# Kernel tuning notes

Hardware: AMD Instinct MI355X
Metric: run time of the kernel (lower is better)

Reference implementation:

```python
import jax, jax.numpy as jnp
import numpy as np

B, C, H, W = 8192, 2048, 2, 2
CR = C // 16
EPS = 1e-5

def setup_inputs() -> dict:
    key = jax.random.key(0)
    ks = jax.random.split(key, 8)
    x = jax.random.normal(ks[0], (B, C, H, W), dtype=jnp.float32)
    gamma = jax.random.normal(ks[1], (C,), dtype=jnp.float32) * 0.1 + 1.0
    beta = jax.random.normal(ks[2], (C,), dtype=jnp.float32) * 0.1
    mean = jax.random.normal(ks[3], (C,), dtype=jnp.float32) * 0.1
    var = jax.random.uniform(ks[4], (C,), dtype=jnp.float32, minval=0.5, maxval=1.5)
    w1 = jax.random.normal(ks[5], (CR, C), dtype=jnp.float32) * (1.0 / np.sqrt(C))
    b1 = jnp.zeros((CR,), dtype=jnp.float32)
    w2 = jax.random.normal(ks[6], (C, CR), dtype=jnp.float32) * (1.0 / np.sqrt(CR))
    b2 = jnp.zeros((C,), dtype=jnp.float32)
    return {"x": x, "gamma": gamma, "beta": beta, "mean": mean, "var": var,
            "w1": w1, "b1": b1, "w2": w2, "b2": b2}

def reference(x, gamma, beta, mean, var, w1, b1, w2, b2):
    # BatchNorm (inference form) + ReLU, over [B,C,H,W]
    inv = gamma * jax.lax.rsqrt(var + EPS)           # [C]
    xn = jax.nn.relu(x * inv[None, :, None, None]
                     + (beta - mean * inv)[None, :, None, None])
    # global average pool -> [B, C]
    p = jnp.mean(xn, axis=(2, 3))
    # two 1x1 convs on [B,C,1,1] == channel MLP
    h = jax.nn.relu(jnp.einsum('bc,rc->br', p, w1) + b1)   # [B, C/16]
    g = jax.nn.sigmoid(jnp.einsum('br,cr->bc', h, w2) + b2) # [B, C]
    # repeat(1,1,2,2) then in-place add == broadcast add over 2x2 spatial
    return x + g[:, :, None, None]
```

## Files before the change

kernel.cpp:

```cpp
#include <hip/hip_runtime.h>


typedef unsigned short u16;
typedef unsigned int u32;
typedef short short8 __attribute__((ext_vector_type(8)));
typedef __bf16 bf16x8 __attribute__((ext_vector_type(8)));
typedef unsigned short ushort4v __attribute__((ext_vector_type(4)));
typedef float floatx4 __attribute__((ext_vector_type(4)));

#define C_CH 2048
#define THREADS 512
#define NB_G 16
#define NB_M 8
#define PROW 2056
#define HROW 136

#define WS_W2_OFF   (128 * 2048)
#define WS_B1_BYTE  (1u << 20)
#define WS_G_BYTE   (2u << 20)
#define WS_SMALL_NEED ((size_t)(1u << 20) + 512 + 2048 * 4)
#define WS_FULL_NEED  ((size_t)(2u << 20) + (size_t)8192 * 2048 * 2)

__device__ __forceinline__ float bf2f(u16 u) {
    u32 v = ((u32)u) << 16;
    return __builtin_bit_cast(float, v);
}
__device__ __forceinline__ u16 f2bf(float f) {
    u32 v = __builtin_bit_cast(u32, f);
    v = (v + 0x7FFFu + ((v >> 16) & 1u)) >> 16;
    return (u16)v;
}
__device__ __forceinline__ bf16x8 ld8(const u16* p) {
    short8 s = *(const short8*)p;
    return __builtin_bit_cast(bf16x8, s);
}
__device__ __forceinline__ bool is_bf16_data(const u16* var_raw) {
    int ok = 1;
    #pragma unroll
    for (int i = 0; i < 8; ++i) {
        u16 u = var_raw[2 * i];
        ok &= (u >= 0x3F00u) && (u <= 0x3FC0u);
    }
    return ok != 0;
}

extern "C" __global__ void __launch_bounds__(256)
se_convw(const void* __restrict__ w1_raw, const void* __restrict__ b1_raw,
         const void* __restrict__ w2_raw, const void* __restrict__ b2_raw,
         const void* __restrict__ var_raw, void* __restrict__ ws) {
    const bool bf = is_bf16_data((const u16*)var_raw);
    u16* w1b = (u16*)ws;
    u16* w2b = w1b + WS_W2_OFF;
    float* b1f = (float*)((char*)ws + WS_B1_BYTE);
    float* b2f = b1f + 128;
    int gid = blockIdx.x * 256 + threadIdx.x;
    if (bf) {
        const ushort4v* s1 = (const ushort4v*)w1_raw;
        const ushort4v* s2 = (const ushort4v*)w2_raw;
        *(ushort4v*)(w1b + gid * 4) = s1[gid];
        *(ushort4v*)(w2b + gid * 4) = s2[gid];
        if (gid < 128)  b1f[gid] = bf2f(((const u16*)b1_raw)[gid]);
        if (gid < 2048) b2f[gid] = bf2f(((const u16*)b2_raw)[gid]);
    } else {
        const floatx4* s1 = (const floatx4*)w1_raw;
        const floatx4* s2 = (const floatx4*)w2_raw;
        floatx4 a = s1[gid], b = s2[gid];
        ushort4v o1, o2;
        #pragma unroll
        for (int j = 0; j < 4; ++j) { o1[j] = f2bf(a[j]); o2[j] = f2bf(b[j]); }
        *(ushort4v*)(w1b + gid * 4) = o1;
        *(ushort4v*)(w2b + gid * 4) = o2;
        if (gid < 128)  b1f[gid] = ((const float*)b1_raw)[gid];
        if (gid < 2048) b2f[gid] = ((const float*)b2_raw)[gid];
    }
}

extern "C" __global__ void __launch_bounds__(THREADS, 4)
se_gate(const void* __restrict__ x_raw,
        const void* __restrict__ gamma_raw,
        const void* __restrict__ beta_raw,
        const void* __restrict__ mean_raw,
        const void* __restrict__ var_raw,
        void* __restrict__ ws) {
    __shared__ u16 p_lds[NB_G * PROW];
    __shared__ u16 h_lds[NB_G * HROW];

    const int tid  = threadIdx.x;
    const int lane = tid & 63;
    const int wv   = tid >> 6;
    const int quad = lane >> 4;
    const int l16  = lane & 15;
    const long b0  = (long)blockIdx.x * NB_G;

    const u16*   w1b = (const u16*)ws;
    const u16*   w2b = w1b + WS_W2_OFF;
    const float* b1f = (const float*)((const char*)ws + WS_B1_BYTE);
    const float* b2f = b1f + 128;
    u16*         g_ws = (u16*)((char*)ws + WS_G_BYTE);

    const bool bf = is_bf16_data((const u16*)var_raw);

    {
        float inv[4], bs[4];
        if (bf) {
            const u16 *gu = (const u16*)gamma_raw, *bu = (const u16*)beta_raw,
                      *mu = (const u16*)mean_raw,  *vu = (const u16*)var_raw;
            #pragma unroll
            for (int k = 0; k < 4; ++k) {
                int c = tid + 512 * k;
                float g = bf2f(gu[c]), bb = bf2f(bu[c]);
                float mm = bf2f(mu[c]), vv = bf2f(vu[c]);
                inv[k] = g * rsqrtf(vv + 1e-5f);
                bs[k]  = bb - mm * inv[k];
            }
        } else {
            const float *gf = (const float*)gamma_raw, *bfp = (const float*)beta_raw,
                        *mf = (const float*)mean_raw,  *vf = (const float*)var_raw;
            #pragma unroll
            for (int k = 0; k < 4; ++k) {
                int c = tid + 512 * k;
                inv[k] = gf[c] * rsqrtf(vf[c] + 1e-5f);
                bs[k]  = bfp[c] - mf[c] * inv[k];
            }
        }
        if (bf) {
            const ushort4v* xr = (const ushort4v*)x_raw + b0 * 2048;
            #pragma unroll 2
            for (int m = 0; m < NB_G; ++m) {
                #pragma unroll
                for (int k = 0; k < 4; ++k) {
                    int c = tid + 512 * k;
                    ushort4v u = xr[m * 2048 + c];
                    float s = 0.f;
                    #pragma unroll
                    for (int j = 0; j < 4; ++j)
                        s += fmaxf(fmaf(bf2f(u[j]), inv[k], bs[k]), 0.f);
                    p_lds[m * PROW + c] = f2bf(s * 0.25f);
                }
            }
        } else {
            const floatx4* xr = (const floatx4*)x_raw + b0 * 2048;
            #pragma unroll 2
            for (int m = 0; m < NB_G; ++m) {
                #pragma unroll
                for (int k = 0; k < 4; ++k) {
                    int c = tid + 512 * k;
                    floatx4 v = xr[m * 2048 + c];
                    float s = 0.f;
                    #pragma unroll
                    for (int j = 0; j < 4; ++j)
                        s += fmaxf(fmaf(v[j], inv[k], bs[k]), 0.f);
                    p_lds[m * PROW + c] = f2bf(s * 0.25f);
                }
            }
        }
    }
    __syncthreads();

    const int rr = (wv << 4) | l16;
    {
        floatx4 acc = {0.f, 0.f, 0.f, 0.f};
        const u16* pp  = p_lds + l16 * PROW + (quad << 3);
        const u16* w1p = w1b + (long)rr * C_CH + (quad << 3);
        #pragma unroll 4
        for (int k0 = 0; k0 < C_CH; k0 += 32)
            acc = __builtin_amdgcn_mfma_f32_16x16x32_bf16(ld8(pp + k0), ld8(w1p + k0), acc, 0, 0, 0);
        float bb = b1f[rr];
        #pragma unroll
        for (int r = 0; r < 4; ++r) {
            int m = (quad << 2) | r;
            h_lds[m * HROW + rr] = f2bf(fmaxf(acc[r] + bb, 0.f));
        }
    }
    __syncthreads();

    {
        bf16x8 af[4];
        #pragma unroll
        for (int kk = 0; kk < 4; ++kk)
            af[kk] = ld8(h_lds + l16 * HROW + (kk << 5) + (quad << 3));

        #pragma unroll 2
        for (int i = 0; i < 16; ++i) {
            int c = (wv * 16 + i) * 16 + l16;
            floatx4 a2 = {0.f, 0.f, 0.f, 0.f};
            const u16* w2p = w2b + (long)c * 128 + (quad << 3);
            #pragma unroll
            for (int kk = 0; kk < 4; ++kk)
                a2 = __builtin_amdgcn_mfma_f32_16x16x32_bf16(af[kk], ld8(w2p + (kk << 5)), a2, 0, 0, 0);
            float zb = b2f[c];
            #pragma unroll
            for (int r = 0; r < 4; ++r) {
                int m = (quad << 2) | r;
                float z = a2[r] + zb;
                float g = 1.f / (1.f + __expf(-z));
                g_ws[(b0 + m) * 2048 + c] = f2bf(g);
            }
        }
    }
}

extern "C" __global__ void __launch_bounds__(THREADS)
se_resid(const void* __restrict__ x_raw,
         const void* __restrict__ var_raw,
         const void* __restrict__ ws,
         void* __restrict__ out_raw) {
    const bool bf = is_bf16_data((const u16*)var_raw);
    const u16* g_ws = (const u16*)((const char*)ws + WS_G_BYTE);
    const int tid = threadIdx.x;

    if (bf) {
        const short8* xr  = (const short8*)x_raw;
        short8*       orr = (short8*)out_raw;
        const long base = (long)blockIdx.x * 4096;
        #pragma unroll 4
        for (int it = 0; it < 8; ++it) {
            long j = base + it * 512 + tid;
            u32 gg = *(const u32*)(g_ws + j * 2);
            float g0 = bf2f((u16)gg), g1 = bf2f((u16)(gg >> 16));
            short8 xv = xr[j];
            short8 ov;
            #pragma unroll
            for (int jj = 0; jj < 4; ++jj) ov[jj] = (short)f2bf(bf2f((u16)xv[jj]) + g0);
            #pragma unroll
            for (int jj = 4; jj < 8; ++jj) ov[jj] = (short)f2bf(bf2f((u16)xv[jj]) + g1);
            __builtin_nontemporal_store(ov, &orr[j]);
        }
    } else {
        const floatx4* xr  = (const floatx4*)x_raw;
        floatx4*       orr = (floatx4*)out_raw;
        const long base = (long)blockIdx.x * 8192;
        #pragma unroll 4
        for (int it = 0; it < 16; ++it) {
            long j = base + it * 512 + tid;
            float g = bf2f(g_ws[j]);
            floatx4 xv = xr[j];
            floatx4 ov = {xv[0] + g, xv[1] + g, xv[2] + g, xv[3] + g};
            __builtin_nontemporal_store(ov, &orr[j]);
        }
    }
}

extern "C" __global__ void __launch_bounds__(THREADS, 8)
se_main(const void* __restrict__ x_raw,
        const void* __restrict__ gamma_raw,
        const void* __restrict__ beta_raw,
        const void* __restrict__ mean_raw,
        const void* __restrict__ var_raw,
        const void* __restrict__ ws,
        void* __restrict__ out_raw) {
    __shared__ u16 p_lds[NB_M * PROW];
    __shared__ u16 h_lds[NB_M * HROW];

    const int tid  = threadIdx.x;
    const int lane = tid & 63;
    const int wv   = tid >> 6;
    const int quad = lane >> 4;
    const int l16  = lane & 15;
    const long b0  = (long)blockIdx.x * NB_M;

    const u16*   w1b = (const u16*)ws;
    const u16*   w2b = w1b + WS_W2_OFF;
    const float* b1f = (const float*)((const char*)ws + WS_B1_BYTE);
    const float* b2f = b1f + 128;

    const bool bf = is_bf16_data((const u16*)var_raw);

    {
        float inv[4], bs[4];
        if (bf) {
            const u16 *gu = (const u16*)gamma_raw, *bu = (const u16*)beta_raw,
                      *mu = (const u16*)mean_raw,  *vu = (const u16*)var_raw;
            #pragma unroll
            for (int k = 0; k < 4; ++k) {
                int c = tid + 512 * k;
                float g = bf2f(gu[c]), bb = bf2f(bu[c]);
                float mm = bf2f(mu[c]), vv = bf2f(vu[c]);
                inv[k] = g * rsqrtf(vv + 1e-5f);
                bs[k]  = bb - mm * inv[k];
            }
        } else {
            const float *gf = (const float*)gamma_raw, *bfp = (const float*)beta_raw,
                        *mf = (const float*)mean_raw,  *vf = (const float*)var_raw;
            #pragma unroll
            for (int k = 0; k < 4; ++k) {
                int c = tid + 512 * k;
                inv[k] = gf[c] * rsqrtf(vf[c] + 1e-5f);
                bs[k]  = bfp[c] - mf[c] * inv[k];
            }
        }
        if (bf) {
            const ushort4v* xr = (const ushort4v*)x_raw + b0 * 2048;
            #pragma unroll 2
            for (int m = 0; m < NB_M; ++m) {
                #pragma unroll
                for (int k = 0; k < 4; ++k) {
                    int c = tid + 512 * k;
                    ushort4v u = xr[m * 2048 + c];
                    float s = 0.f;
                    #pragma unroll
                    for (int j = 0; j < 4; ++j)
                        s += fmaxf(fmaf(bf2f(u[j]), inv[k], bs[k]), 0.f);
                    p_lds[m * PROW + c] = f2bf(s * 0.25f);
                }
            }
        } else {
            const floatx4* xr = (const floatx4*)x_raw + b0 * 2048;
            #pragma unroll 2
            for (int m = 0; m < NB_M; ++m) {
                #pragma unroll
                for (int k = 0; k < 4; ++k) {
                    int c = tid + 512 * k;
                    floatx4 v = xr[m * 2048 + c];
                    float s = 0.f;
                    #pragma unroll
                    for (int j = 0; j < 4; ++j)
                        s += fmaxf(fmaf(v[j], inv[k], bs[k]), 0.f);
                    p_lds[m * PROW + c] = f2bf(s * 0.25f);
                }
            }
        }
    }
    __syncthreads();

    const int rr = (wv << 4) | l16;
    {
        floatx4 acc = {0.f, 0.f, 0.f, 0.f};
        const u16* pp  = p_lds + (l16 & 7) * PROW + (quad << 3);
        const u16* w1p = w1b + (long)rr * C_CH + (quad << 3);
        #pragma unroll 4
        for (int k0 = 0; k0 < C_CH; k0 += 32)
            acc = __builtin_amdgcn_mfma_f32_16x16x32_bf16(ld8(pp + k0), ld8(w1p + k0), acc, 0, 0, 0);
        float bb = b1f[rr];
        if (quad < 2) {
            #pragma unroll
            for (int r = 0; r < 4; ++r) {
                int m = (quad << 2) | r;
                h_lds[m * HROW + rr] = f2bf(fmaxf(acc[r] + bb, 0.f));
            }
        }
    }
    __syncthreads();

    {
        bf16x8 af[4];
        #pragma unroll
        for (int kk = 0; kk < 4; ++kk)
            af[kk] = ld8(h_lds + (l16 & 7) * HROW + (kk << 5) + (quad << 3));

        #pragma unroll 2
        for (int i = 0; i < 16; ++i) {
            int c = (wv * 16 + i) * 16 + l16;
            floatx4 a2 = {0.f, 0.f, 0.f, 0.f};
            const u16* w2p = w2b + (long)c * 128 + (quad << 3);
            #pragma unroll
            for (int kk = 0; kk < 4; ++kk)
                a2 = __builtin_amdgcn_mfma_f32_16x16x32_bf16(af[kk], ld8(w2p + (kk << 5)), a2, 0, 0, 0);
            float zb = b2f[c];
            if (quad < 2) {
                #pragma unroll
                for (int r = 0; r < 4; ++r) {
                    int m = (quad << 2) | r;
                    float z = a2[r] + zb;
                    float g = 1.f / (1.f + __expf(-z));
                    p_lds[m * PROW + c] = f2bf(g);
                }
            }
        }
    }
    __syncthreads();

    if (bf) {
        const short8* xr8 = (const short8*)x_raw + b0 * 1024;
        short8*       or8 = (short8*)out_raw + b0 * 1024;
        #pragma unroll 4
        for (int it = 0; it < 16; ++it) {
            int j  = (it << 9) | tid;
            int m  = j >> 10, cc = j & 1023;
            u32 gg = *(const u32*)(&p_lds[m * PROW + (cc << 1)]);
            float g0 = bf2f((u16)gg), g1 = bf2f((u16)(gg >> 16));
            short8 xv = __builtin_nontemporal_load(&xr8[j]);
            short8 ov;
            #pragma unroll
            for (int jj = 0; jj < 4; ++jj) ov[jj] = (short)f2bf(bf2f((u16)xv[jj]) + g0);
            #pragma unroll
            for (int jj = 4; jj < 8; ++jj) ov[jj] = (short)f2bf(bf2f((u16)xv[jj]) + g1);
            __builtin_nontemporal_store(ov, &or8[j]);
        }
    } else {
        const floatx4* xr = (const floatx4*)x_raw + b0 * 2048;
        floatx4*       orr = (floatx4*)out_raw + b0 * 2048;
        #pragma unroll 4
        for (int it = 0; it < 32; ++it) {
            int j = (it << 9) | tid;
            int m = j >> 11, c = j & 2047;
            float g = bf2f(p_lds[m * PROW + c]);
            floatx4 xv = __builtin_nontemporal_load(&xr[j]);
            floatx4 ov = {xv[0] + g, xv[1] + g, xv[2] + g, xv[3] + g};
            __builtin_nontemporal_store(ov, &orr[j]);
        }
    }
}

extern "C" void kernel_launch(void* const* d_in, const int* in_sizes, int n_in,
                              void* d_out, int out_size, void* d_ws, size_t ws_size,
                              hipStream_t stream) {
    se_convw<<<dim3(256), dim3(256), 0, stream>>>(
        d_in[5], d_in[6], d_in[7], d_in[8], d_in[4], d_ws);
    if (d_ws != nullptr && ws_size >= WS_FULL_NEED) {
        se_gate<<<dim3(8192 / NB_G), dim3(THREADS), 0, stream>>>(
            d_in[0], d_in[1], d_in[2], d_in[3], d_in[4], d_ws);
        se_resid<<<dim3(2048), dim3(THREADS), 0, stream>>>(
            d_in[0], d_in[4], d_ws, d_out);
    } else {
        se_main<<<dim3(8192 / NB_M), dim3(THREADS), 0, stream>>>(
            d_in[0], d_in[1], d_in[2], d_in[3], d_in[4], d_ws, d_out);
    }
}
```

Measured before the change: 559.3 us.

## Split fused gate kernel into streaming pool kernel and 64-row tiled MLP kernel

```diff
diff --git a/kernel.cpp b/kernel.cpp
--- a/kernel.cpp
+++ b/kernel.cpp
@@ -10,16 +10,15 @@
 
 #define C_CH 2048
 #define THREADS 512
-#define NB_G 16
 #define NB_M 8
 #define PROW 2056
 #define HROW 136
 
 #define WS_W2_OFF   (128 * 2048)
 #define WS_B1_BYTE  (1u << 20)
-#define WS_G_BYTE   (2u << 20)
-#define WS_SMALL_NEED ((size_t)(1u << 20) + 512 + 2048 * 4)
-#define WS_FULL_NEED  ((size_t)(2u << 20) + (size_t)8192 * 2048 * 2)
+#define WS_P_BYTE   (2u << 20)
+#define WS_G_BYTE   ((2u << 20) + (32u << 20))
+#define WS_FULL_NEED ((size_t)(2u << 20) + 2 * (size_t)(32u << 20))
 
 __device__ __forceinline__ float bf2f(u16 u) {
     u32 v = ((u32)u) << 16;
@@ -75,126 +74,145 @@
     }
 }
 
-extern "C" __global__ void __launch_bounds__(THREADS, 4)
-se_gate(const void* __restrict__ x_raw,
+extern "C" __global__ void __launch_bounds__(THREADS)
+se_pool(const void* __restrict__ x_raw,
         const void* __restrict__ gamma_raw,
         const void* __restrict__ beta_raw,
         const void* __restrict__ mean_raw,
         const void* __restrict__ var_raw,
         void* __restrict__ ws) {
-    __shared__ u16 p_lds[NB_G * PROW];
-    __shared__ u16 h_lds[NB_G * HROW];
+    const bool bf = is_bf16_data((const u16*)var_raw);
+    u16* p_ws = (u16*)((char*)ws + WS_P_BYTE);
+    const int tid = threadIdx.x;
+
+    float inv[4], bs[4];
+    if (bf) {
+        const u16 *gu = (const u16*)gamma_raw, *bu = (const u16*)beta_raw,
+                  *mu = (const u16*)mean_raw,  *vu = (const u16*)var_raw;
+        #pragma unroll
+        for (int k = 0; k < 4; ++k) {
+            int c = tid + 512 * k;
+            float g = bf2f(gu[c]), bb = bf2f(bu[c]);
+            float mm = bf2f(mu[c]), vv = bf2f(vu[c]);
+            inv[k] = g * rsqrtf(vv + 1e-5f);
+            bs[k]  = bb - mm * inv[k];
+        }
+    } else {
+        const float *gf = (const float*)gamma_raw, *bfp = (const float*)beta_raw,
+                    *mf = (const float*)mean_raw,  *vf = (const float*)var_raw;
+        #pragma unroll
+        for (int k = 0; k < 4; ++k) {
+            int c = tid + 512 * k;
+            inv[k] = gf[c] * rsqrtf(vf[c] + 1e-5f);
+            bs[k]  = bfp[c] - mf[c] * inv[k];
+        }
+    }
+
+    const long base = (long)blockIdx.x * 8192;
+    if (bf) {
+        const ushort4v* xr = (const ushort4v*)x_raw;
+        #pragma unroll 4
+        for (int it = 0; it < 16; ++it) {
+            long j = base + it * 512 + tid;
+            int k = it & 3;
+            ushort4v u = __builtin_nontemporal_load(&xr[j]);
+            float s = 0.f;
+            #pragma unroll
+            for (int jj = 0; jj < 4; ++jj)
+                s += fmaxf(fmaf(bf2f(u[jj]), inv[k], bs[k]), 0.f);
+            p_ws[j] = f2bf(s * 0.25f);
+        }
+    } else {
+        const floatx4* xr = (const floatx4*)x_raw;
+        #pragma unroll 4
+        for (int it = 0; it < 16; ++it) {
+            long j = base + it * 512 + tid;
+            int k = it & 3;
+            floatx4 v = __builtin_nontemporal_load(&xr[j]);
+            float s = 0.f;
+            #pragma unroll
+            for (int jj = 0; jj < 4; ++jj)
+                s += fmaxf(fmaf(v[jj], inv[k], bs[k]), 0.f);
+            p_ws[j] = f2bf(s * 0.25f);
+        }
+    }
+}
+
+extern "C" __global__ void __launch_bounds__(THREADS)
+se_mlp(void* __restrict__ ws) {
+    __shared__ u16 h_lds[64 * HROW];
 
     const int tid  = threadIdx.x;
     const int lane = tid & 63;
     const int wv   = tid >> 6;
     const int quad = lane >> 4;
     const int l16  = lane & 15;
-    const long b0  = (long)blockIdx.x * NB_G;
+    const long r0  = (long)blockIdx.x * 64;
 
     const u16*   w1b = (const u16*)ws;
     const u16*   w2b = w1b + WS_W2_OFF;
     const float* b1f = (const float*)((const char*)ws + WS_B1_BYTE);
     const float* b2f = b1f + 128;
+    const u16*   p_ws = (const u16*)((const char*)ws + WS_P_BYTE);
     u16*         g_ws = (u16*)((char*)ws + WS_G_BYTE);
 
-    const bool bf = is_bf16_data((const u16*)var_raw);
-
+    const int wv_m = wv & 3;
+    const int wv_n = wv >> 2;
     {
-        float inv[4], bs[4];
-        if (bf) {
-            const u16 *gu = (const u16*)gamma_raw, *bu = (const u16*)beta_raw,
-                      *mu = (const u16*)mean_raw,  *vu = (const u16*)var_raw;
-            #pragma unroll
-            for (int k = 0; k < 4; ++k) {
-                int c = tid + 512 * k;
-                float g = bf2f(gu[c]), bb = bf2f(bu[c]);
-                float mm = bf2f(mu[c]), vv = bf2f(vu[c]);
-                inv[k] = g * rsqrtf(vv + 1e-5f);
-                bs[k]  = bb - mm * inv[k];
-            }
-        } else {
-            const float *gf = (const float*)gamma_raw, *bfp = (const float*)beta_raw,
-                        *mf = (const float*)mean_raw,  *vf = (const float*)var_raw;
-            #pragma unroll
-            for (int k = 0; k < 4; ++k) {
-                int c = tid + 512 * k;
-                inv[k] = gf[c] * rsqrtf(vf[c] + 1e-5f);
-                bs[k]  = bfp[c] - mf[c] * inv[k];
-            }
-        }
-        if (bf) {
-            const ushort4v* xr = (const ushort4v*)x_raw + b0 * 2048;
-            #pragma unroll 2
-            for (int m = 0; m < NB_G; ++m) {
+        floatx4 acc[4] = {{0.f,0.f,0.f,0.f},{0.f,0.f,0.f,0.f},
+                          {0.f,0.f,0.f,0.f},{0.f,0.f,0.f,0.f}};
+        const u16* ap = p_ws + (r0 + wv_m * 16 + l16) * 2048 + (quad << 3);
+        const u16* bp = w1b + (long)(wv_n * 64 + l16) * 2048 + (quad << 3);
+        #pragma unroll 2
+        for (int k0 = 0; k0 < C_CH; k0 += 32) {
+            bf16x8 a = ld8(ap + k0);
+            #pragma unroll
+            for (int nt = 0; nt < 4; ++nt)
+                acc[nt] = __builtin_amdgcn_mfma_f32_16x16x32_bf16(
+                    a, ld8(bp + nt * 16 * 2048 + k0), acc[nt], 0, 0, 0);
+        }
+        #pragma unroll
+        for (int nt = 0; nt < 4; ++nt) {
+            int col = wv_n * 64 + nt * 16 + l16;
+            float bb = b1f[col];
+            #pragma unroll
+            for (int r = 0; r < 4; ++r) {
+                int row = wv_m * 16 + (quad << 2) + r;
+                h_lds[row * HROW + col] = f2bf(fmaxf(acc[nt][r] + bb, 0.f));
+            }
+        }
+    }
+    __syncthreads();
+
+    {
+        bf16x8 af[4][4];
+        #pragma unroll
+        for (int mt = 0; mt < 4; ++mt)
+            #pragma unroll
+            for (int ks = 0; ks < 4; ++ks)
+                af[mt][ks] = ld8(h_lds + (mt * 16 + l16) * HROW + (ks << 5) + (quad << 3));
+
+        const int n0 = wv << 8;
+        for (int nt2 = 0; nt2 < 16; ++nt2) {
+            int n = n0 + nt2 * 16;
+            const u16* w2p = w2b + (long)(n + l16) * 128 + (quad << 3);
+            bf16x8 bw[4];
+            #pragma unroll
+            for (int ks = 0; ks < 4; ++ks) bw[ks] = ld8(w2p + (ks << 5));
+            float zb = b2f[n + l16];
+            #pragma unroll
+            for (int mt = 0; mt < 4; ++mt) {
+                floatx4 ac = {0.f, 0.f, 0.f, 0.f};
                 #pragma unroll
-                for (int k = 0; k < 4; ++k) {
-                    int c = tid + 512 * k;
-                    ushort4v u = xr[m * 2048 + c];
-                    float s = 0.f;
-                    #pragma unroll
-                    for (int j = 0; j < 4; ++j)
-                        s += fmaxf(fmaf(bf2f(u[j]), inv[k], bs[k]), 0.f);
-                    p_lds[m * PROW + c] = f2bf(s * 0.25f);
+                for (int ks = 0; ks < 4; ++ks)
+                    ac = __builtin_amdgcn_mfma_f32_16x16x32_bf16(af[mt][ks], bw[ks], ac, 0, 0, 0);
+                #pragma unroll
+                for (int r = 0; r < 4; ++r) {
+                    long row = r0 + mt * 16 + (quad << 2) + r;
+                    float z = ac[r] + zb;
+                    float g = 1.f / (1.f + __expf(-z));
+                    g_ws[row * 2048 + n + l16] = f2bf(g);
                 }
-            }
-        } else {
-            const floatx4* xr = (const floatx4*)x_raw + b0 * 2048;
-            #pragma unroll 2
-            for (int m = 0; m < NB_G; ++m) {
-                #pragma unroll
-                for (int k = 0; k < 4; ++k) {
-                    int c = tid + 512 * k;
-                    floatx4 v = xr[m * 2048 + c];
-                    float s = 0.f;
-                    #pragma unroll
-                    for (int j = 0; j < 4; ++j)
-                        s += fmaxf(fmaf(v[j], inv[k], bs[k]), 0.f);
-                    p_lds[m * PROW + c] = f2bf(s * 0.25f);
-                }
-            }
-        }
-    }
-    __syncthreads();
-
-    const int rr = (wv << 4) | l16;
-    {
-        floatx4 acc = {0.f, 0.f, 0.f, 0.f};
-        const u16* pp  = p_lds + l16 * PROW + (quad << 3);
-        const u16* w1p = w1b + (long)rr * C_CH + (quad << 3);
-        #pragma unroll 4
-        for (int k0 = 0; k0 < C_CH; k0 += 32)
-            acc = __builtin_amdgcn_mfma_f32_16x16x32_bf16(ld8(pp + k0), ld8(w1p + k0), acc, 0, 0, 0);
-        float bb = b1f[rr];
-        #pragma unroll
-        for (int r = 0; r < 4; ++r) {
-            int m = (quad << 2) | r;
-            h_lds[m * HROW + rr] = f2bf(fmaxf(acc[r] + bb, 0.f));
-        }
-    }
-    __syncthreads();
-
-    {
-        bf16x8 af[4];
-        #pragma unroll
-        for (int kk = 0; kk < 4; ++kk)
-            af[kk] = ld8(h_lds + l16 * HROW + (kk << 5) + (quad << 3));
-
-        #pragma unroll 2
-        for (int i = 0; i < 16; ++i) {
-            int c = (wv * 16 + i) * 16 + l16;
-            floatx4 a2 = {0.f, 0.f, 0.f, 0.f};
-            const u16* w2p = w2b + (long)c * 128 + (quad << 3);
-            #pragma unroll
-            for (int kk = 0; kk < 4; ++kk)
-                a2 = __builtin_amdgcn_mfma_f32_16x16x32_bf16(af[kk], ld8(w2p + (kk << 5)), a2, 0, 0, 0);
-            float zb = b2f[c];
-            #pragma unroll
-            for (int r = 0; r < 4; ++r) {
-                int m = (quad << 2) | r;
-                float z = a2[r] + zb;
-                float g = 1.f / (1.f + __expf(-z));
-                g_ws[(b0 + m) * 2048 + c] = f2bf(g);
             }
         }
     }
@@ -218,7 +236,7 @@
             long j = base + it * 512 + tid;
             u32 gg = *(const u32*)(g_ws + j * 2);
             float g0 = bf2f((u16)gg), g1 = bf2f((u16)(gg >> 16));
-            short8 xv = xr[j];
+            short8 xv = __builtin_nontemporal_load(&xr[j]);
             short8 ov;
             #pragma unroll
             for (int jj = 0; jj < 4; ++jj) ov[jj] = (short)f2bf(bf2f((u16)xv[jj]) + g0);
@@ -234,7 +252,7 @@
         for (int it = 0; it < 16; ++it) {
             long j = base + it * 512 + tid;
             float g = bf2f(g_ws[j]);
-            floatx4 xv = xr[j];
+            floatx4 xv = __builtin_nontemporal_load(&xr[j]);
             floatx4 ov = {xv[0] + g, xv[1] + g, xv[2] + g, xv[3] + g};
             __builtin_nontemporal_store(ov, &orr[j]);
         }
@@ -408,8 +426,9 @@
     se_convw<<<dim3(256), dim3(256), 0, stream>>>(
         d_in[5], d_in[6], d_in[7], d_in[8], d_in[4], d_ws);
     if (d_ws != nullptr && ws_size >= WS_FULL_NEED) {
-        se_gate<<<dim3(8192 / NB_G), dim3(THREADS), 0, stream>>>(
+        se_pool<<<dim3(2048), dim3(THREADS), 0, stream>>>(
             d_in[0], d_in[1], d_in[2], d_in[3], d_in[4], d_ws);
+        se_mlp<<<dim3(128), dim3(THREADS), 0, stream>>>(d_ws);
         se_resid<<<dim3(2048), dim3(THREADS), 0, stream>>>(
             d_in[0], d_in[4], d_ws, d_out);
     } else {
```

Result: slower. 595.3 us (+6.4%).
